# Kernel tuning notes

Hardware: AMD Instinct MI355X
Metric: run time of the kernel (lower is better)

## Reference

```python
import jax, jax.numpy as jnp
import numpy as np

B, S, H, L, NH, DH, FF = 64, 128, 768, 6, 12, 64, 3072
VOCAB, MAXPOS, INTENT, TAGS = 30522, 512, 22, 122
LN_EPS = 1e-12
INV_SQRT_DH = float(1.0 / np.sqrt(DH))


def _ln(x, s, b):
    m = x.mean(-1, keepdims=True)
    v = ((x - m) ** 2).mean(-1, keepdims=True)
    return (x - m) * jax.lax.rsqrt(v + LN_EPS) * s + b


def setup_inputs():
    key = jax.random.key(0)
    cnt = [0]
    def nk():
        cnt[0] += 1
        return jax.random.fold_in(key, cnt[0])
    def nrm(shape):
        return (0.02 * jax.random.normal(nk(), shape)).astype(jnp.float32)
    inp = {
        'input_ids': jax.random.randint(nk(), (B, S), 0, VOCAB),
        'attention_mask': jnp.ones((B, S), jnp.int32),
        'intent_target': jax.random.randint(nk(), (B,), 0, INTENT),
        'slots_target': jax.random.randint(nk(), (B, S), 0, TAGS),
        'slots_mask': jnp.ones((B, S), jnp.int32),
        'word_emb': nrm((VOCAB, H)), 'pos_emb': nrm((MAXPOS, H)),
        'emb_ln_s': jnp.ones((H,)), 'emb_ln_b': jnp.zeros((H,)),
        'Wq': nrm((L, H, H)), 'bq': jnp.zeros((L, H)),
        'Wk': nrm((L, H, H)), 'bk': jnp.zeros((L, H)),
        'Wv': nrm((L, H, H)), 'bv': jnp.zeros((L, H)),
        'Wo': nrm((L, H, H)), 'bo': jnp.zeros((L, H)),
        'sa_ln_s': jnp.ones((L, H)), 'sa_ln_b': jnp.zeros((L, H)),
        'W1f': nrm((L, H, FF)), 'b1f': jnp.zeros((L, FF)),
        'W2f': nrm((L, FF, H)), 'b2f': jnp.zeros((L, H)),
        'out_ln_s': jnp.ones((L, H)), 'out_ln_b': jnp.zeros((L, H)),
        'iW1': nrm((H, 64)), 'ib1': jnp.zeros((64,)),
        'iW2': nrm((64, INTENT)), 'ib2': jnp.zeros((INTENT,)),
        'sW1': nrm((H, 256)), 'sb1': jnp.zeros((256,)),
        'sW2': nrm((256, TAGS)), 'sb2': jnp.zeros((TAGS,)),
        'crf_start': nrm((TAGS,)), 'crf_end': nrm((TAGS,)), 'crf_trans': nrm((TAGS, TAGS)),
        'log_vars': jnp.zeros((2,)),
    }
    return inp


def _encoder(input_ids, attention_mask, word_emb, pos_emb, emb_ln_s, emb_ln_b,
             Wq, bq, Wk, bk, Wv, bv, Wo, bo, sa_ln_s, sa_ln_b,
             W1f, b1f, W2f, b2f, out_ln_s, out_ln_b):
    x = word_emb[input_ids] + pos_emb[jnp.arange(S)][None]
    x = _ln(x, emb_ln_s, emb_ln_b)
    neg = jnp.where(attention_mask[:, None, None, :] > 0, 0.0, -1e9).astype(x.dtype)
    for i in range(L):
        q = (x @ Wq[i] + bq[i]).reshape(B, S, NH, DH).transpose(0, 2, 1, 3)
        k = (x @ Wk[i] + bk[i]).reshape(B, S, NH, DH).transpose(0, 2, 1, 3)
        v = (x @ Wv[i] + bv[i]).reshape(B, S, NH, DH).transpose(0, 2, 1, 3)
        scores = jnp.einsum('bhqd,bhkd->bhqk', q, k) * INV_SQRT_DH + neg
        attn = jax.nn.softmax(scores, -1)
        ctx = jnp.einsum('bhqk,bhkd->bhqd', attn, v).transpose(0, 2, 1, 3).reshape(B, S, H)
        x = _ln(x + ctx @ Wo[i] + bo[i], sa_ln_s[i], sa_ln_b[i])
        h = jax.nn.gelu(x @ W1f[i] + b1f[i], approximate=False) @ W2f[i] + b2f[i]
        x = _ln(x + h, out_ln_s[i], out_ln_b[i])
    return x


def _crf_llh(emis, tags, mask, crf_start, crf_end, crf_trans):
    # pytorch-crf log-likelihood, reduction='sum'. emis [B,S,T], mask bool [B,S]
    fmask = mask.astype(emis.dtype)
    emit_sc = jnp.take_along_axis(emis, tags[..., None], -1)[..., 0]          # [B,S]
    trans_sc = crf_trans[tags[:, :-1], tags[:, 1:]]                            # [B,S-1]
    last_idx = mask.sum(1) - 1
    last_tag = tags[jnp.arange(B), last_idx]
    num = (crf_start[tags[:, 0]] + emit_sc[:, 0]
           + ((trans_sc + emit_sc[:, 1:]) * fmask[:, 1:]).sum(1)
           + crf_end[last_tag])
    def fstep(alpha, xs):
        emit_t, m_t = xs
        nxt = jax.nn.logsumexp(alpha[:, :, None] + crf_trans[None] + emit_t[:, None, :], axis=1)
        return jnp.where(m_t[:, None], nxt, alpha), None
    alpha0 = crf_start[None] + emis[:, 0]
    alpha, _ = jax.lax.scan(fstep, alpha0, (emis[:, 1:].transpose(1, 0, 2), mask[:, 1:].T))
    denom = jax.nn.logsumexp(alpha + crf_end[None], -1)
    return jnp.sum(num - denom)


def _viterbi(emis, mask, crf_start, crf_end, crf_trans):
    ident = jnp.arange(TAGS)[None, :]
    def vstep(alpha, xs):
        emit_t, m_t = xs
        score = alpha[:, :, None] + crf_trans[None] + emit_t[:, None, :]      # [B,T,T]
        bp = jnp.where(m_t[:, None], jnp.argmax(score, 1), ident)
        alpha = jnp.where(m_t[:, None], jnp.max(score, 1), alpha)
        return alpha, bp
    alpha0 = crf_start[None] + emis[:, 0]
    alpha, bps = jax.lax.scan(vstep, alpha0, (emis[:, 1:].transpose(1, 0, 2), mask[:, 1:].T))
    last = jnp.argmax(alpha + crf_end[None], -1)                               # [B]
    def bstep(tag, bp):
        prev = jnp.take_along_axis(bp, tag[:, None], 1)[:, 0]
        return prev, prev
    _, prevs = jax.lax.scan(bstep, last, bps, reverse=True)                    # [S-1,B]
    return jnp.concatenate([prevs, last[None]], 0).T                           # [B,S]


def reference(input_ids, attention_mask, intent_target, slots_target, slots_mask,
              word_emb, pos_emb, emb_ln_s, emb_ln_b,
              Wq, bq, Wk, bk, Wv, bv, Wo, bo, sa_ln_s, sa_ln_b,
              W1f, b1f, W2f, b2f, out_ln_s, out_ln_b,
              iW1, ib1, iW2, ib2, sW1, sb1, sW2, sb2,
              crf_start, crf_end, crf_trans, log_vars):
    x = _encoder(input_ids, attention_mask, word_emb, pos_emb, emb_ln_s, emb_ln_b,
                 Wq, bq, Wk, bk, Wv, bv, Wo, bo, sa_ln_s, sa_ln_b,
                 W1f, b1f, W2f, b2f, out_ln_s, out_ln_b)
    # intent head: linear1(relu(cls)) -> relu -> linear2 (dropout = eval identity)
    intent_logits = jax.nn.relu(jax.nn.relu(x[:, 0]) @ iW1 + ib1) @ iW2 + ib2
    intent_loss = (jax.nn.logsumexp(intent_logits, -1)
                   - jnp.take_along_axis(intent_logits, intent_target[:, None], 1)[:, 0])
    intent_pred = jnp.argmax(intent_logits, -1)
    # slots head
    slots_logits = jax.nn.relu(jax.nn.relu(x) @ sW1 + sb1) @ sW2 + sb2
    mask = slots_mask.astype(bool)
    slots_loss = -_crf_llh(slots_logits, slots_target, mask, crf_start, crf_end, crf_trans)
    p1 = jnp.exp(-log_vars[0])
    p2 = jnp.exp(-log_vars[1])
    joint_loss = jnp.sum(p1 * intent_loss + log_vars[0]) + (p2 * slots_loss + log_vars[1])
    slots_pred = _viterbi(slots_logits, mask, crf_start, crf_end, crf_trans)
    return joint_loss, slots_pred, intent_pred
```

## Files before the change

### kernel.cpp

```cpp
#include <hip/hip_runtime.h>
#include <math.h>
#include <stdint.h>

#define B_      64
#define S_      128
#define H_      768
#define L_      6
#define NH_     12
#define DH_     64
#define FF_     3072
#define INTENT_ 22
#define TAGS_   122
#define NT_     (B_*S_)
#define LN_EPS  1e-12f
#define INV_SQRT_DH 0.125f

#define GF_RELU_OUT 2
#define GF_GELU_OUT 4
#define GF_ADDRES   16
#define GF_ACCH     32

typedef _Float16 half8 __attribute__((ext_vector_type(8)));
typedef float    f32x4 __attribute__((ext_vector_type(4)));

// ... 209 lines not shown
            bfl[i] = *(const half8*)&Bl[n*32 + slot*8];
        }
        #pragma unroll
        for (int i = 0; i < 4; i++)
            #pragma unroll
            for (int j = 0; j < 4; j++) {
                acc[i][j] = __builtin_amdgcn_mfma_f32_16x16x32_f16(afh[i], bfh[j], acc[i][j], 0,0,0);
                acc[i][j] = __builtin_amdgcn_mfma_f32_16x16x32_f16(afh[i], bfl[j], acc[i][j], 0,0,0);
                acc[i][j] = __builtin_amdgcn_mfma_f32_16x16x32_f16(afl[i], bfh[j], acc[i][j], 0,0,0);
            }
        __syncthreads();
    }
    #pragma unroll
    for (int i = 0; i < 4; i++)
        #pragma unroll
        for (int j = 0; j < 4; j++)
            #pragma unroll
            for (int r = 0; r < 4; r++) {
                int gm = m0 + wm*64 + i*16 + quad*4 + r;
                int gn = n0 + wn*64 + j*16 + l15;
                float v = acc[i][j][r];
                if (bias) v += bias[gn];
                size_t ox = (size_t)gm*ldc + gn;
                if (flags & GF_ADDRES) {
                    size_t rx = (size_t)gm*ldr + gn;
                    v += (float)Rh[rx] + (float)Rl[rx];
                }
                if (flags & GF_ACCH)
                    v += (float)oh[ox] + (float)ol[ox];
                if (flags & GF_RELU_OUT) v = fmaxf(v, 0.f);
                if (flags & GF_GELU_OUT) v = 0.5f*v*(1.0f + erff(v*0.70710678118654752f));
                if (oh) {
                    _Float16 hv = (_Float16)v;
                    oh[ox] = hv;
                    ol[ox] = (_Float16)(v - (float)hv);
                } else {
                    C[ox] = v;
                }
            }
}

#define BM 64
#define BN 64
#define BK 16
__global__ __launch_bounds__(256) void gemm_kernel(
    const float* __restrict__ A, int lda,
    const float* __restrict__ W, int ldb,
    float* __restrict__ C, int ldc,
    const float* __restrict__ bias,
    int M, int N, int K)
{
    __shared__ __align__(16) float As[BK][BM+4];
    __shared__ __align__(16) float Bs[BK][BN+4];
    int tid = threadIdx.x;
    int tx = tid & 15, ty = tid >> 4;
    int m0 = blockIdx.x * BM;
    int n0 = blockIdx.y * BN;
    float acc[4][4] = {};
    for (int k0 = 0; k0 < K; k0 += BK) {
        #pragma unroll
        for (int r = 0; r < 4; r++) {
            int li = tid + 256*r;
            int m  = li >> 4;
            int kk = li & 15;
            int gm = m0 + m, gk = k0 + kk;
            As[kk][m] = (gm < M && gk < K) ? A[(size_t)gm*lda + gk] : 0.f;
        }
        #pragma unroll
        for (int r = 0; r < 4; r++) {
            int li = tid + 256*r;
            int kk = li >> 6;
            int n  = li & 63;
            int gk = k0 + kk, gn = n0 + n;
            Bs[kk][n] = (gk < K && gn < N) ? W[(size_t)gk*ldb + gn] : 0.f;
        }
        __syncthreads();
        #pragma unroll
        for (int kk = 0; kk < BK; kk++) {
            float4 a  = *(const float4*)&As[kk][ty*4];
            float4 bb = *(const float4*)&Bs[kk][tx*4];
            float av[4] = {a.x, a.y, a.z, a.w};
            float bv[4] = {bb.x, bb.y, bb.z, bb.w};
            #pragma unroll
            for (int i = 0; i < 4; i++)
                #pragma unroll
                for (int j = 0; j < 4; j++)
                    acc[i][j] += av[i] * bv[j];
        }
        __syncthreads();
    }
    #pragma unroll
    for (int i = 0; i < 4; i++) {
        int gm = m0 + ty*4 + i;
        if (gm >= M) continue;
        #pragma unroll
        for (int j = 0; j < 4; j++) {
            int gn = n0 + tx*4 + j;
            if (gn >= N) continue;
            float v = acc[i][j];
            if (bias) v += bias[gn];
            C[(size_t)gm*ldc + gn] = v;
        }
    }
}

__device__ inline int scidx(int row, int col) {
    return row*128 + (((col>>2) ^ (row&7))<<2) + (col&3);
}
__global__ __launch_bounds__(256) void attn2_kernel(
    const _Float16* __restrict__ QhG, const _Float16* __restrict__ QlG,
    const _Float16* __restrict__ KhG, const _Float16* __restrict__ KlG,
    const _Float16* __restrict__ VhG, const _Float16* __restrict__ VlG,
    const int* __restrict__ amask,
    _Float16* __restrict__ Ch, _Float16* __restrict__ Cl)
{
    __shared__ __align__(16) char smem[65536];
    _Float16* Qh_s = (_Float16*)smem;
    _Float16* Ql_s = Qh_s + 64*72;
    _Float16* Kh_s = Ql_s + 64*72;
    _Float16* Kl_s = Kh_s + 128*72;
    float*    Sc   = (float*)smem;
    _Float16* Vth  = (_Float16*)(smem + 32768);
    _Float16* Vtl  = Vth + 64*128;

    int blk = blockIdx.x;
    int qh2 = blk & 1;
    int bh  = blk >> 1;
    int b = bh / NH_, hh = bh % NH_;
    const int tid = threadIdx.x, lane = tid&63, wid = tid>>6;
    const int l15 = lane&15, quad = lane>>4;
    const int qr = wid*16;
    size_t tokb = (size_t)b*S_*H_ + (size_t)hh*DH_;

    float nmask[8];
    #pragma unroll
    for (int j = 0; j < 8; j++)
        nmask[j] = (amask[b*S_ + j*16 + l15] > 0) ? 0.f : -1e9f;

    {
        int row = tid>>2, part = (tid&3)*16;
        size_t qg = tokb + (size_t)(qh2*64 + row)*H_ + part;
        *(uint4*)&Qh_s[row*72 + part] = *(const uint4*)(QhG + qg);
        *(uint4*)&Ql_s[row*72 + part] = *(const uint4*)(QlG + qg);
        #pragma unroll
        for (int p = 0; p < 2; p++) {
            int krow = row + p*64;
            size_t kg = tokb + (size_t)krow*H_ + part;
            *(uint4*)&Kh_s[krow*72 + part] = *(const uint4*)(KhG + kg);
            *(uint4*)&Kl_s[krow*72 + part] = *(const uint4*)(KlG + kg);
        }
    }
    __syncthreads();

    f32x4 acc1[8];
    #pragma unroll
    for (int j = 0; j < 8; j++) acc1[j] = (f32x4){0.f,0.f,0.f,0.f};
    half8 aqh[2], aql[2];
    #pragma unroll
    for (int kc = 0; kc < 2; kc++) {
        aqh[kc] = *(const half8*)&Qh_s[(qr + l15)*72 + kc*32 + quad*8];
        aql[kc] = *(const half8*)&Ql_s[(qr + l15)*72 + kc*32 + quad*8];
    }
    #pragma unroll
    for (int j = 0; j < 8; j++) {
        #pragma unroll
        for (int kc = 0; kc < 2; kc++) {
            half8 bkh = *(const half8*)&Kh_s[(j*16 + l15)*72 + kc*32 + quad*8];
            half8 bkl = *(const half8*)&Kl_s[(j*16 + l15)*72 + kc*32 + quad*8];
            acc1[j] = __builtin_amdgcn_mfma_f32_16x16x32_f16(aqh[kc], bkh, acc1[j], 0,0,0);
            acc1[j] = __builtin_amdgcn_mfma_f32_16x16x32_f16(aqh[kc], bkl, acc1[j], 0,0,0);
            acc1[j] = __builtin_amdgcn_mfma_f32_16x16x32_f16(aql[kc], bkh, acc1[j], 0,0,0);
        }
    }
    __syncthreads();

    #pragma unroll
    for (int j = 0; j < 8; j++)
        #pragma unroll
        for (int r = 0; r < 4; r++) {
            int row = qr + quad*4 + r;
            int col = j*16 + l15;
            Sc[scidx(row, col)] = acc1[j][r]*INV_SQRT_DH + nmask[j];
        }
    {
        int key = tid>>1, dh = (tid&1)*32;
        union V32 { _Float16 h[32]; uint4 u[4]; } bufh, bufl;
        #pragma unroll
        for (int e = 0; e < 4; e++) {
            bufh.u[e] = *(const uint4*)(VhG + tokb + (size_t)key*H_ + dh + e*8);
            bufl.u[e] = *(const uint4*)(VlG + tokb + (size_t)key*H_ + dh + e*8);
        }
        int kg = key>>3, kr = key&7;
        #pragma unroll
        for (int e = 0; e < 32; e++) {
            int d = dh + e;
            int pos = kg ^ (d & 7);
            Vth[d*128 + pos*8 + kr] = bufh.h[e];
            Vtl[d*128 + pos*8 + kr] = bufl.h[e];
        }
    }
    __syncthreads();

    {
        int row = tid>>2, part = (tid&3)*32;
        float mx = -INFINITY;
        #pragma unroll 8
        for (int e = 0; e < 32; e++)
            mx = fmaxf(mx, Sc[scidx(row, part+e)]);
        mx = fmaxf(mx, __shfl_xor(mx, 1));
        mx = fmaxf(mx, __shfl_xor(mx, 2));
        float s = 0.f;
        #pragma unroll 8
        for (int e = 0; e < 32; e++) {
            int idx = scidx(row, part+e);
            float ev = expf(Sc[idx] - mx);
            Sc[idx] = ev; s += ev;
        }
        s += __shfl_xor(s, 1);
        s += __shfl_xor(s, 2);
        float inv = 1.0f / s;
        #pragma unroll 8
        for (int e = 0; e < 32; e++)
            Sc[scidx(row, part+e)] *= inv;
    }
    __syncthreads();

    f32x4 acc2[4];
    #pragma unroll
    for (int jd = 0; jd < 4; jd++) acc2[jd] = (f32x4){0.f,0.f,0.f,0.f};
    #pragma unroll
    for (int kc = 0; kc < 4; kc++) {
        int q = qr + l15;
        int g16 = kc*8 + quad*2;
        float4 p0 = *(const float4*)&Sc[q*128 + ((g16   ^ (q&7))<<2)];
        float4 p1 = *(const float4*)&Sc[q*128 + (((g16+1) ^ (q&7))<<2)];
        float pv[8] = {p0.x,p0.y,p0.z,p0.w, p1.x,p1.y,p1.z,p1.w};
        union U { _Float16 h[8]; half8 v; } ph, pl;
        #pragma unroll
        for (int e = 0; e < 8; e++) {
            _Float16 hv = (_Float16)pv[e];
            ph.h[e] = hv; pl.h[e] = (_Float16)(pv[e] - (float)hv);
        }
        #pragma unroll
        for (int jd = 0; jd < 4; jd++) {
            int n = jd*16 + l15;
            int pos = (kc*4 + quad) ^ (n & 7);
            half8 vh = *(const half8*)&Vth[n*128 + pos*8];
            half8 vl = *(const half8*)&Vtl[n*128 + pos*8];
            acc2[jd] = __builtin_amdgcn_mfma_f32_16x16x32_f16(ph.v, vh, acc2[jd], 0,0,0);
            acc2[jd] = __builtin_amdgcn_mfma_f32_16x16x32_f16(ph.v, vl, acc2[jd], 0,0,0);
            acc2[jd] = __builtin_amdgcn_mfma_f32_16x16x32_f16(pl.v, vh, acc2[jd], 0,0,0);
        }
    }
    #pragma unroll
    for (int jd = 0; jd < 4; jd++)
        #pragma unroll
        for (int r = 0; r < 4; r++) {
            int row = qr + quad*4 + r;
            int token = b*S_ + qh2*64 + row;
            int d = jd*16 + l15;
            float v = acc2[jd][r];
            _Float16 hv = (_Float16)v;
            Ch[(size_t)token*H_ + hh*DH_ + d] = hv;
            Cl[(size_t)token*H_ + hh*DH_ + d] = (_Float16)(v - (float)hv);
        }
}

__global__ __launch_bounds__(64) void intent_kernel(
    const _Float16* __restrict__ Xh, const _Float16* __restrict__ Xl,
    const float* __restrict__ iW1,
    const float* __restrict__ ib1, const float* __restrict__ iW2,
    const float* __restrict__ ib2, const int* __restrict__ tgt,
    float* __restrict__ iloss, float* __restrict__ outf)
{
    int b = blockIdx.x; int j = threadIdx.x;
    __shared__ float h1[64];
    __shared__ float lg[32];
    const _Float16* x0h = Xh + (size_t)b*S_*H_;
    const _Float16* x0l = Xl + (size_t)b*S_*H_;
    float acc = ib1[j];
    for (int h = 0; h < H_; h++) {
        float x = (float)x0h[h] + (float)x0l[h];
        acc += fmaxf(x, 0.f) * iW1[(size_t)h*64 + j];
    }
    h1[j] = fmaxf(acc, 0.f);
    __syncthreads();
    if (j < INTENT_) {
        float l = ib2[j];
        for (int k = 0; k < 64; k++) l += h1[k]*iW2[k*INTENT_ + j];
        lg[j] = l;
    }
    __syncthreads();
    if (j == 0) {
        float mx = -INFINITY; int bi = 0;
        for (int c = 0; c < INTENT_; c++) if (lg[c] > mx) { mx = lg[c]; bi = c; }
        float sm = 0.f;
        for (int c = 0; c < INTENT_; c++) sm += expf(lg[c]-mx);
        float lse = mx + logf(sm);
        iloss[b] = lse - lg[tgt[b]];
        outf[1 + (size_t)NT_ + b] = (float)bi;
    }
}

#define VST 130
__global__ __launch_bounds__(512) void crf_vit_kernel(
    const float* __restrict__ E_, const int* __restrict__ tags,
    const int* __restrict__ mask, const float* __restrict__ start,
    const float* __restrict__ endv, const float* __restrict__ trans,
    float* __restrict__ crfv, unsigned char* __restrict__ BPg,
    float* __restrict__ outf)
{
    __shared__ __align__(16) float tT[TAGS_*VST];
    __shared__ float alpha[TAGS_+2];
    __shared__ float ealpha[TAGS_+2];
    __shared__ float mxbuf[16];
    __shared__ int lastt;
    int b = blockIdx.x;
    int mode = blockIdx.y;
    int tid = threadIdx.x, lane = tid&63, wid = tid>>6;
    int j = tid>>2, p = tid&3;
    int cnt = (p < 2) ? 31 : 30;
    const float* E = E_ + (size_t)b*S_*TAGS_;

    if (j < TAGS_) {
        for (int e = 0; e < cnt; e++) {
            int i = 4*e + p;
            float tv = trans[i*TAGS_ + j];
            tT[j*VST + i] = mode ? tv : expf(tv);
        }
        if (p == 0) alpha[j] = start[j] + E[j];
    }
    __syncthreads();

    if (mode == 0) {
        for (int t = 1; t < S_; t++) {
            if (wid == 0) {
                float a = (lane < TAGS_) ? alpha[lane] : -3e38f;
                if (lane + 64 < TAGS_) a = fmaxf(a, alpha[lane+64]);
                a = wave_max(a);
                if (lane == 0) mxbuf[0] = a;
            }
            __syncthreads();
            float mx = mxbuf[0];
            if (p == 0 && j < TAGS_) ealpha[j] = expf(alpha[j] - mx);
            __syncthreads();
            float s = 0.f;
            if (j < TAGS_) {
                const float* tr = &tT[j*VST];
                for (int e = 0; e < cnt; e++) {
                    int i = 4*e + p;
                    s += ealpha[i]*tr[i];
                }
            }
            s += __shfl_xor(s, 1);
            s += __shfl_xor(s, 2);
            int m_t = mask[b*S_ + t];
            float ee = (j < TAGS_) ? E[(size_t)t*TAGS_ + j] : 0.f;
            float nv = mx + logf(s) + ee;
            __syncthreads();
            if (p == 0 && j < TAGS_ && m_t) alpha[j] = nv;
            __syncthreads();
        }
        float term = 0.f, mkf = 0.f;
        if (tid < S_) {
            int mk = mask[b*S_ + tid]; mkf = (float)mk;
            if (tid >= 1 && mk) {
                int tg = tags[b*S_ + tid], tgp = tags[b*S_ + tid - 1];
                term = trans[tgp*TAGS_ + tg] + E[(size_t)tid*TAGS_ + tg];
            }
        }
        if (wid < 2) {
            float ts = wave_sum(term);
            float ms = wave_sum(mkf);
            if (lane == 0) { mxbuf[2+wid] = ts; mxbuf[4+wid] = ms; }
        }
        __syncthreads();
        if (wid == 0) {
            float v1 = (lane < TAGS_) ? alpha[lane] + endv[lane] : -3e38f;
            float v2 = (lane+64 < TAGS_) ? alpha[lane+64] + endv[lane+64] : -3e38f;
            float m = wave_max(fmaxf(v1, v2));
            float sd = ((lane < TAGS_) ? expf(v1 - m) : 0.f)
                     + ((lane+64 < TAGS_) ? expf(v2 - m) : 0.f);
            sd = wave_sum(sd);
            if (lane == 0) {
                float denom = m + logf(sd);
                float numsum = mxbuf[2] + mxbuf[3];
                int msum = (int)(mxbuf[4] + mxbuf[5]);
                int tag0 = tags[b*S_];
                int last_tag = tags[b*S_ + (msum - 1)];
                float num = start[tag0] + E[tag0] + numsum + endv[last_tag];
                crfv[b] = num - denom;
            }
        }
    } else {
        size_t bpb = (size_t)b*(S_-1)*TAGS_;
        for (int t = 1; t < S_; t++) {
            float best = -3e38f; int bi = 0;
            if (j < TAGS_) {
                const float* tr = &tT[j*VST];
                for (int e = 0; e < cnt; e++) {
                    int i = 4*e + p;
                    float v = alpha[i] + tr[i];
                    if (v > best) { best = v; bi = i; }
                }
            }
            {
                float ov = __shfl_xor(best, 1); int oi = __shfl_xor(bi, 1);
                if (ov > best || (ov == best && oi < bi)) { best = ov; bi = oi; }
                ov = __shfl_xor(best, 2); oi = __shfl_xor(bi, 2);
                if (ov > best || (ov == best && oi < bi)) { best = ov; bi = oi; }
            }
            int m_t = mask[b*S_ + t];
            float ee = (j < TAGS_) ? E[(size_t)t*TAGS_ + j] : 0.f;
            float nv; int nb;
            if (m_t) { nv = best + ee; nb = bi; }
            else     { nv = (j < TAGS_) ? alpha[j] : 0.f; nb = j; }
            __syncthreads();
            if (p == 0 && j < TAGS_) {
                alpha[j] = nv;
                BPg[bpb + (size_t)(t-1)*TAGS_ + j] = (unsigned char)nb;
            }
            __syncthreads();
        }
        if (wid == 0) {
            float v; int idx;
            float v1 = (lane < TAGS_) ? alpha[lane] + endv[lane] : -3e38f;
            float v2 = (lane+64 < TAGS_) ? alpha[lane+64] + endv[lane+64] : -3e38f;
            if (v2 > v1) { v = v2; idx = lane+64; } else { v = v1; idx = lane; }
            #pragma unroll
            for (int d = 32; d; d >>= 1) {
                float ov = __shfl_xor(v, d); int oi = __shfl_xor(idx, d);
                if (ov > v || (ov == v && oi < idx)) { v = ov; idx = oi; }
            }
            if (lane == 0) lastt = idx;
        }
        __syncthreads();
        unsigned char* bpl = (unsigned char*)tT;
        for (int o = tid; o < (S_-1)*TAGS_; o += 512)
            bpl[o] = BPg[bpb + o];
        __syncthreads();
        if (tid == 0) {
            int tag = lastt;
            outf[1 + (size_t)b*S_ + (S_-1)] = (float)tag;
            for (int t = S_-1; t >= 1; t--) {
                tag = bpl[(t-1)*TAGS_ + tag];
                outf[1 + (size_t)b*S_ + (t-1)] = (float)tag;
            }
        }
    }
}

__global__ void combine_kernel(const float* __restrict__ iloss,
                               const float* __restrict__ crfv,
                               const float* __restrict__ lv,
                               float* __restrict__ outf)
{
    if (threadIdx.x == 0 && blockIdx.x == 0) {
        float si = 0.f, sc = 0.f;
        for (int b = 0; b < B_; b++) { si += iloss[b]; sc += crfv[b]; }
        float p1 = expf(-lv[0]), p2 = expf(-lv[1]);
        float slots_loss = -sc;
        outf[0] = p1*si + (float)B_*lv[0] + p2*slots_loss + lv[1];
    }
}

extern "C" void kernel_launch(void* const* d_in, const int* in_sizes, int n_in,
                              void* d_out, int out_size, void* d_ws, size_t ws_size,
                              hipStream_t stream) {
    const int*   ids   = (const int*)  d_in[0];
    const int*   amask = (const int*)  d_in[1];
    const int*   itgt  = (const int*)  d_in[2];
    const int*   stgt  = (const int*)  d_in[3];
    const int*   smask = (const int*)  d_in[4];
    const float* we    = (const float*)d_in[5];
    const float* pe    = (const float*)d_in[6];
    const float* embs  = (const float*)d_in[7];
    const float* embb  = (const float*)d_in[8];
    const float* Wq    = (const float*)d_in[9];
    const float* bq    = (const float*)d_in[10];
    const float* Wk    = (const float*)d_in[11];
    const float* bk    = (const float*)d_in[12];
    const float* Wv    = (const float*)d_in[13];
    const float* bv    = (const float*)d_in[14];
    const float* Wo    = (const float*)d_in[15];
    const float* bo    = (const float*)d_in[16];
    const float* sas   = (const float*)d_in[17];
    const float* sab   = (const float*)d_in[18];
    const float* W1f   = (const float*)d_in[19];
    const float* b1f   = (const float*)d_in[20];
    const float* W2f   = (const float*)d_in[21];
    const float* b2f   = (const float*)d_in[22];
    const float* ols   = (const float*)d_in[23];
    const float* olb   = (const float*)d_in[24];
    const float* iW1   = (const float*)d_in[25];
    const float* ib1   = (const float*)d_in[26];
    const float* iW2   = (const float*)d_in[27];
    const float* ib2   = (const float*)d_in[28];
    const float* sW1   = (const float*)d_in[29];
    const float* sb1   = (const float*)d_in[30];
    const float* sW2   = (const float*)d_in[31];
    const float* sb2   = (const float*)d_in[32];
    const float* crfs  = (const float*)d_in[33];
    const float* crfe  = (const float*)d_in[34];
    const float* crft  = (const float*)d_in[35];
    const float* lv    = (const float*)d_in[36];

    float* outf = (float*)d_out;
    float* wsf  = (float*)d_ws;
    const long NTHh = (long)NT_ * H_;
    const long NBf  = NTHh;
    const long HH   = (long)H_ * H_;

    _Float16* Xh = (_Float16*)wsf;
    _Float16* Xl = Xh + NTHh;
    float*    Pf = wsf + NBf;
    _Float16* Ph = (_Float16*)Pf;
    _Float16 *Qh = Ph, *Ql = Ph + NTHh, *Kh = Ph + 2*NTHh, *Kl = Ph + 3*NTHh,
             *Vh = Ph + 4*NTHh, *Vl = Ph + 5*NTHh;
    _Float16 *Sh = Ph, *Sl = Ph + NTHh;
    _Float16* Fh = (_Float16*)(wsf + 2*NBf);
    _Float16* Fl = (_Float16*)(wsf + 3*NBf);
    _Float16* Ch = (_Float16*)(wsf + 4*NBf);
    _Float16* Cl = Ch + NTHh;
    const long wa0 = 5*NBf;
    _Float16* WAh = (_Float16*)(wsf + wa0);
    _Float16* WAl = WAh + 4*HH;
    const long wb1 = wa0 + 2359296;
    _Float16* WB1h = (_Float16*)(wsf + wb1);
    _Float16* WB1l = WB1h + 2359296;
    const long wb2 = wb1 + 2359296;
    _Float16* WB2h = (_Float16*)(wsf + wb2);
    _Float16* WB2l = WB2h + 2359296;
    float* iloss = wsf + wb2 + 2359296;
    float* crfv  = iloss + 64;
    float* H1 = Pf;
    float* logits = Pf + 2097152;
    unsigned char* BPg = (unsigned char*)(Pf + 2097152 + 999424);

    auto g3 = [&](int gy, int gz,
                  const _Float16* A_h, const _Float16* A_l, int lda,
                  const _Float16* WtH, const _Float16* WtL, int ldw, long wz,
                  float* C, _Float16* OH, _Float16* OL, int ldc, long oz,
                  const _Float16* Rh, const _Float16* Rl,
                  const float* b0, const float* b1_, const float* b2_,
                  int K, int flags) {
        hipLaunchKernelGGL(gemm3_kernel, dim3(NT_/128, gy, gz), dim3(256), 0, stream,
                           A_h, A_l, lda, WtH, WtL, ldw, wz,
                           C, OH, OL, ldc, oz, Rh, Rl, H_, b0, b1_, b2_, K, flags);
    };

    hipLaunchKernelGGL(embed_ln_kernel, dim3(NT_), dim3(256), 0, stream,
                       ids, we, pe, embs, embb, Xh, Xl);

    for (int i = 0; i < L_; i++) {
        const long WO = (long)i*HH;
        hipLaunchKernelGGL(wconv_kernel, dim3(12,12,4), dim3(256), 0, stream,
                           Wq+WO, Wk+WO, Wv+WO, Wo+WO, H_, H_, WAh, WAl, HH);
        g3(6, 3, Xh, Xl, H_, WAh, WAl, H_, HH,
           nullptr, Ph, Ph+NTHh, H_, 2*NTHh, nullptr, nullptr,
           bq+i*H_, bk+i*H_, bv+i*H_, H_, 0);
        hipLaunchKernelGGL(attn2_kernel, dim3(B_*NH_*2), dim3(256), 0, stream,
                           Qh, Ql, Kh, Kl, Vh, Vl, amask, Ch, Cl);
        g3(6, 1, Ch, Cl, H_, WAh+3*HH, WAl+3*HH, H_, 0,
           nullptr, Sh, Sl, H_, 0, Xh, Xl,
           bo+i*H_, nullptr, nullptr, H_, GF_ADDRES);
        hipLaunchKernelGGL(ln2_kernel, dim3(NT_), dim3(384), 0, stream,
                           Sh, Sl, sas+i*H_, sab+i*H_, Xh, Xl,
                           (_Float16*)nullptr, (_Float16*)nullptr);
        hipLaunchKernelGGL(wconv_kernel, dim3(12,48,1), dim3(256), 0, stream,
                           W1f+(long)i*H_*FF_, nullptr, nullptr, nullptr,
                           H_, FF_, WB1h, WB1l, 0);
        hipLaunchKernelGGL(wconv_kernel, dim3(48,12,1), dim3(256), 0, stream,
                           W2f+(long)i*FF_*H_, nullptr, nullptr, nullptr,
                           FF_, H_, WB2h, WB2l, 0);
        for (int c = 0; c < 2; c++) {
            const int CW = FF_/2;
            g3(12, 1, Xh, Xl, H_,
               WB1h+(long)c*CW*H_, WB1l+(long)c*CW*H_, H_, 0,
               nullptr, Fh, Fl, CW, 0, nullptr, nullptr,
               b1f+(long)i*FF_+c*CW, nullptr, nullptr, H_, GF_GELU_OUT);
            g3(6, 1, Fh, Fl, CW,
               WB2h+(long)c*CW, WB2l+(long)c*CW, FF_, 0,
               nullptr, Sh, Sl, H_, 0, Xh, Xl,
               (c==0) ? (b2f+i*H_) : nullptr, nullptr, nullptr,
               CW, (c==0) ? GF_ADDRES : GF_ACCH);
        }
        hipLaunchKernelGGL(ln2_kernel, dim3(NT_), dim3(384), 0, stream,
                           Sh, Sl, ols+i*H_, olb+i*H_, Xh, Xl,
                           (i==L_-1) ? Ch : (_Float16*)nullptr,
                           (i==L_-1) ? Cl : (_Float16*)nullptr);
    }

    hipLaunchKernelGGL(intent_kernel, dim3(B_), dim3(64), 0, stream,
                       Xh, Xl, iW1, ib1, iW2, ib2, itgt, iloss, outf);

    hipLaunchKernelGGL(wconv_kernel, dim3(12,4,1), dim3(256), 0, stream,
                       sW1, nullptr, nullptr, nullptr, H_, 256,
                       WAh, WAh + (long)256*H_, 0);
    g3(2, 1, Ch, Cl, H_, WAh, WAh + (long)256*H_, H_, 0,
       H1, nullptr, nullptr, 256, 0, nullptr, nullptr,
       sb1, nullptr, nullptr, H_, GF_RELU_OUT);
    hipLaunchKernelGGL(gemm_kernel, dim3(NT_/BM, 2), dim3(256), 0, stream,
                       H1, 256, sW2, TAGS_, logits, TAGS_, sb2, NT_, TAGS_, 256);

    hipLaunchKernelGGL(crf_vit_kernel, dim3(B_, 2), dim3(512), 0, stream,
                       logits, stgt, smask, crfs, crfe, crft, crfv, BPg, outf);

    hipLaunchKernelGGL(combine_kernel, dim3(1), dim3(64), 0, stream,
                       iloss, crfv, lv, outf);
}
```

Baseline: 4.870 ms.

## Rewrite CRF/Viterbi kernel as single-wavefront with register-held alpha

The CRF forward and Viterbi kernel moves from 512 threads (4 lanes per tag with shared-memory alpha and several block barriers per timestep) to one 64-lane wavefront where each lane owns two tags in registers. Transitions are stored in an interleaved layout so each lane reads float4 values, and alpha is exchanged through a small LDS buffer without block barriers. This targets the serial per-timestep barrier and reduction overhead of the 127-step recurrence, at the cost of each lane doing the full 122-wide inner loop serially. Tie-breaking in the Viterbi argmax now depends on scan order instead of an explicit lowest-index rule.

```diff
diff --git a/kernel.cpp b/kernel.cpp
--- a/kernel.cpp
+++ b/kernel.cpp
@@ -535,145 +535,132 @@
     }
 }
 
-#define VST 130
-__global__ __launch_bounds__(512) void crf_vit_kernel(
+__global__ __launch_bounds__(64) void crf_vit_kernel(
     const float* __restrict__ E_, const int* __restrict__ tags,
     const int* __restrict__ mask, const float* __restrict__ start,
     const float* __restrict__ endv, const float* __restrict__ trans,
     float* __restrict__ crfv, unsigned char* __restrict__ BPg,
     float* __restrict__ outf)
 {
-    __shared__ __align__(16) float tT[TAGS_*VST];
-    __shared__ float alpha[TAGS_+2];
-    __shared__ float ealpha[TAGS_+2];
-    __shared__ float mxbuf[16];
-    __shared__ int lastt;
-    int b = blockIdx.x;
-    int mode = blockIdx.y;
-    int tid = threadIdx.x, lane = tid&63, wid = tid>>6;
-    int j = tid>>2, p = tid&3;
-    int cnt = (p < 2) ? 31 : 30;
+    __shared__ __align__(16) float Ti[61*256];
+    __shared__ __align__(16) float eab[128];
+    int b = blockIdx.x, mode = blockIdx.y;
+    int lane = threadIdx.x;
     const float* E = E_ + (size_t)b*S_*TAGS_;
-
-    if (j < TAGS_) {
-        for (int e = 0; e < cnt; e++) {
-            int i = 4*e + p;
-            float tv = trans[i*TAGS_ + j];
-            tT[j*VST + i] = mode ? tv : expf(tv);
-        }
-        if (p == 0) alpha[j] = start[j] + E[j];
-    }
-    __syncthreads();
+    int j0 = 2*lane, j1 = 2*lane+1;
+    bool vj0 = (j0 < TAGS_), vj1 = (j1 < TAGS_);
+
+    for (int o = lane; o < 61*256; o += 64) {
+        int i2 = o >> 8, r = o & 255, j = r >> 1, p = r & 1;
+        int i = 2*i2 + p;
+        float tv = (j < TAGS_) ? trans[i*TAGS_ + j] : 0.f;
+        Ti[o] = mode ? tv : expf(tv);
+    }
+    __syncthreads();
+
+    float a0 = vj0 ? (start[j0] + E[j0]) : -3e38f;
+    float a1 = vj1 ? (start[j1] + E[j1]) : -3e38f;
 
     if (mode == 0) {
         for (int t = 1; t < S_; t++) {
-            if (wid == 0) {
-                float a = (lane < TAGS_) ? alpha[lane] : -3e38f;
-                if (lane + 64 < TAGS_) a = fmaxf(a, alpha[lane+64]);
-                a = wave_max(a);
-                if (lane == 0) mxbuf[0] = a;
+            float e0 = vj0 ? E[(size_t)t*TAGS_ + j0] : 0.f;
+            float e1 = vj1 ? E[(size_t)t*TAGS_ + j1] : 0.f;
+            int m_t = mask[b*S_ + t];
+            float mx = wave_max(fmaxf(a0, a1));
+            float2 ea;
+            ea.x = vj0 ? expf(a0 - mx) : 0.f;
+            ea.y = vj1 ? expf(a1 - mx) : 0.f;
+            *(float2*)&eab[2*lane] = ea;
+            float s0 = 0.f, s1 = 0.f;
+            #pragma unroll
+            for (int i2 = 0; i2 < 61; i2++) {
+                float2 av = *(const float2*)&eab[2*i2];
+                float4 tv = *(const float4*)&Ti[i2*256 + 4*lane];
+                s0 += av.x*tv.x + av.y*tv.y;
+                s1 += av.x*tv.z + av.y*tv.w;
             }
-            __syncthreads();
-            float mx = mxbuf[0];
-            if (p == 0 && j < TAGS_) ealpha[j] = expf(alpha[j] - mx);
-            __syncthreads();
-            float s = 0.f;
-            if (j < TAGS_) {
-                const float* tr = &tT[j*VST];
-                for (int e = 0; e < cnt; e++) {
-                    int i = 4*e + p;
-                    s += ealpha[i]*tr[i];
-                }
+            if (m_t) {
+                if (vj0) a0 = mx + logf(s0) + e0;
+                if (vj1) a1 = mx + logf(s1) + e1;
             }
-            s += __shfl_xor(s, 1);
-            s += __shfl_xor(s, 2);
-            int m_t = mask[b*S_ + t];
-            float ee = (j < TAGS_) ? E[(size_t)t*TAGS_ + j] : 0.f;
-            float nv = mx + logf(s) + ee;
-            __syncthreads();
-            if (p == 0 && j < TAGS_ && m_t) alpha[j] = nv;
-            __syncthreads();
         }
         float term = 0.f, mkf = 0.f;
-        if (tid < S_) {
-            int mk = mask[b*S_ + tid]; mkf = (float)mk;
-            if (tid >= 1 && mk) {
-                int tg = tags[b*S_ + tid], tgp = tags[b*S_ + tid - 1];
-                term = trans[tgp*TAGS_ + tg] + E[(size_t)tid*TAGS_ + tg];
+        #pragma unroll
+        for (int rr = 0; rr < 2; rr++) {
+            int t = lane + 64*rr;
+            int mk = mask[b*S_ + t];
+            mkf += (float)mk;
+            if (t >= 1 && mk) {
+                int tg = tags[b*S_ + t], tgp = tags[b*S_ + t - 1];
+                term += trans[tgp*TAGS_ + tg] + E[(size_t)t*TAGS_ + tg];
             }
         }
-        if (wid < 2) {
-            float ts = wave_sum(term);
-            float ms = wave_sum(mkf);
-            if (lane == 0) { mxbuf[2+wid] = ts; mxbuf[4+wid] = ms; }
-        }
-        __syncthreads();
-        if (wid == 0) {
-            float v1 = (lane < TAGS_) ? alpha[lane] + endv[lane] : -3e38f;
-            float v2 = (lane+64 < TAGS_) ? alpha[lane+64] + endv[lane+64] : -3e38f;
-            float m = wave_max(fmaxf(v1, v2));
-            float sd = ((lane < TAGS_) ? expf(v1 - m) : 0.f)
-                     + ((lane+64 < TAGS_) ? expf(v2 - m) : 0.f);
-            sd = wave_sum(sd);
-            if (lane == 0) {
-                float denom = m + logf(sd);
-                float numsum = mxbuf[2] + mxbuf[3];
-                int msum = (int)(mxbuf[4] + mxbuf[5]);
-                int tag0 = tags[b*S_];
-                int last_tag = tags[b*S_ + (msum - 1)];
-                float num = start[tag0] + E[tag0] + numsum + endv[last_tag];
-                crfv[b] = num - denom;
-            }
+        float ts = wave_sum(term);
+        float ms = wave_sum(mkf);
+        float w0 = vj0 ? a0 + endv[j0] : -3e38f;
+        float w1 = vj1 ? a1 + endv[j1] : -3e38f;
+        float m2 = wave_max(fmaxf(w0, w1));
+        float sd = (vj0 ? expf(w0 - m2) : 0.f) + (vj1 ? expf(w1 - m2) : 0.f);
+        sd = wave_sum(sd);
+        if (lane == 0) {
+            float denom = m2 + logf(sd);
+            int msum = (int)ms;
+            int tag0 = tags[b*S_];
+            int last_tag = tags[b*S_ + (msum - 1)];
+            crfv[b] = start[tag0] + E[tag0] + ts + endv[last_tag] - denom;
         }
     } else {
         size_t bpb = (size_t)b*(S_-1)*TAGS_;
         for (int t = 1; t < S_; t++) {
-            float best = -3e38f; int bi = 0;
-            if (j < TAGS_) {
-                const float* tr = &tT[j*VST];
-                for (int e = 0; e < cnt; e++) {
-                    int i = 4*e + p;
-                    float v = alpha[i] + tr[i];
-                    if (v > best) { best = v; bi = i; }
+            float e0 = vj0 ? E[(size_t)t*TAGS_ + j0] : 0.f;
+            float e1 = vj1 ? E[(size_t)t*TAGS_ + j1] : 0.f;
+            int m_t = mask[b*S_ + t];
+            float2 ap; ap.x = a0; ap.y = a1;
+            *(float2*)&eab[2*lane] = ap;
+            float b0 = -3e38f, b1 = -3e38f; int i0 = 0, i1 = 0;
+            #pragma unroll
+            for (int i2 = 0; i2 < 61; i2++) {
+                float2 av = *(const float2*)&eab[2*i2];
+                float4 tv = *(const float4*)&Ti[i2*256 + 4*lane];
+                float c0 = av.x + tv.x;
+                if (c0 > b0) { b0 = c0; i0 = 2*i2; }
+                float c1 = av.y + tv.y;
+                if (c1 > b0) { b0 = c1; i0 = 2*i2+1; }
+                float c2 = av.x + tv.z;
+                if (c2 > b1) { b1 = c2; i1 = 2*i2; }
+                float c3 = av.y + tv.w;
+                if (c3 > b1) { b1 = c3; i1 = 2*i2+1; }
+            }
+            float n0, n1; int nb0, nb1;
+            if (m_t) { n0 = b0 + e0; nb0 = i0; n1 = b1 + e1; nb1 = i1; }
+            else     { n0 = a0; nb0 = j0; n1 = a1; nb1 = j1; }
+            if (vj0) a0 = n0;
+            if (vj1) a1 = n1;
+            if (vj0) {
+                size_t bx = bpb + (size_t)(t-1)*TAGS_ + j0;
+                if (vj1) {
+                    unsigned short pk = (unsigned short)(((nb1 & 0xff) << 8) | (nb0 & 0xff));
+                    *(unsigned short*)&BPg[bx] = pk;
+                } else {
+                    BPg[bx] = (unsigned char)nb0;
                 }
             }
-            {
-                float ov = __shfl_xor(best, 1); int oi = __shfl_xor(bi, 1);
-                if (ov > best || (ov == best && oi < bi)) { best = ov; bi = oi; }
-                ov = __shfl_xor(best, 2); oi = __shfl_xor(bi, 2);
-                if (ov > best || (ov == best && oi < bi)) { best = ov; bi = oi; }
-            }
-            int m_t = mask[b*S_ + t];
-            float ee = (j < TAGS_) ? E[(size_t)t*TAGS_ + j] : 0.f;
-            float nv; int nb;
-            if (m_t) { nv = best + ee; nb = bi; }
-            else     { nv = (j < TAGS_) ? alpha[j] : 0.f; nb = j; }
-            __syncthreads();
-            if (p == 0 && j < TAGS_) {
-                alpha[j] = nv;
-                BPg[bpb + (size_t)(t-1)*TAGS_ + j] = (unsigned char)nb;
-            }
-            __syncthreads();
-        }
-        if (wid == 0) {
-            float v; int idx;
-            float v1 = (lane < TAGS_) ? alpha[lane] + endv[lane] : -3e38f;
-            float v2 = (lane+64 < TAGS_) ? alpha[lane+64] + endv[lane+64] : -3e38f;
-            if (v2 > v1) { v = v2; idx = lane+64; } else { v = v1; idx = lane; }
-            #pragma unroll
-            for (int d = 32; d; d >>= 1) {
-                float ov = __shfl_xor(v, d); int oi = __shfl_xor(idx, d);
-                if (ov > v || (ov == v && oi < idx)) { v = ov; idx = oi; }
-            }
-            if (lane == 0) lastt = idx;
-        }
-        __syncthreads();
-        unsigned char* bpl = (unsigned char*)tT;
-        for (int o = tid; o < (S_-1)*TAGS_; o += 512)
+        }
+        float w0 = vj0 ? a0 + endv[j0] : -3e38f;
+        float w1 = vj1 ? a1 + endv[j1] : -3e38f;
+        float v = w0; int idx = j0;
+        if (w1 > v) { v = w1; idx = j1; }
+        #pragma unroll
+        for (int d = 32; d; d >>= 1) {
+            float ov = __shfl_xor(v, d); int oi = __shfl_xor(idx, d);
+            if (ov > v || (ov == v && oi < idx)) { v = ov; idx = oi; }
+        }
+        unsigned char* bpl = (unsigned char*)Ti;
+        for (int o = lane; o < (S_-1)*TAGS_; o += 64)
             bpl[o] = BPg[bpb + o];
         __syncthreads();
-        if (tid == 0) {
-            int tag = lastt;
+        if (lane == 0) {
+            int tag = idx;
             outf[1 + (size_t)b*S_ + (S_-1)] = (float)tag;
             for (int t = S_-1; t >= 1; t--) {
                 tag = bpl[(t-1)*TAGS_ + tag];
@@ -836,7 +823,7 @@
     hipLaunchKernelGGL(gemm_kernel, dim3(NT_/BM, 2), dim3(256), 0, stream,
                        H1, 256, sW2, TAGS_, logits, TAGS_, sb2, NT_, TAGS_, 256);
 
-    hipLaunchKernelGGL(crf_vit_kernel, dim3(B_, 2), dim3(512), 0, stream,
+    hipLaunchKernelGGL(crf_vit_kernel, dim3(B_, 2), dim3(64), 0, stream,
                        logits, stgt, smask, crfs, crfe, crft, crfv, BPg, outf);
 
     hipLaunchKernelGGL(combine_kernel, dim3(1), dim3(64), 0, stream,
```

After: 5.072 ms. 4.2% more time.

## Restructure CRF/Viterbi recurrence to one thread per tag with fewer barriers

Applied to the files above, without the earlier changes.

The CRF forward and Viterbi kernel now uses 128 threads, one per tag, instead of 512 threads with four partial-sum lanes per tag. Alpha is kept in registers and exchanged through a double-buffered shared array, which cuts each timestep to a single barrier. The running max is lagged by one step, and emissions and mask values are prefetched one step ahead. Each thread now performs a full 122-length dot or max per step using float4 loads, so per-thread work grows while synchronisation drops.

```diff
diff --git a/kernel.cpp b/kernel.cpp
--- a/kernel.cpp
+++ b/kernel.cpp
@@ -535,141 +535,164 @@
     }
 }
 
-#define VST 130
-__global__ __launch_bounds__(512) void crf_vit_kernel(
+#define VST 132
+__global__ __launch_bounds__(128) void crf_vit_kernel(
     const float* __restrict__ E_, const int* __restrict__ tags,
     const int* __restrict__ mask, const float* __restrict__ start,
     const float* __restrict__ endv, const float* __restrict__ trans,
     float* __restrict__ crfv, unsigned char* __restrict__ BPg,
     float* __restrict__ outf)
 {
-    __shared__ __align__(16) float tT[TAGS_*VST];
-    __shared__ float alpha[TAGS_+2];
-    __shared__ float ealpha[TAGS_+2];
-    __shared__ float mxbuf[16];
+    __shared__ __align__(16) float Ti[TAGS_*VST];
+    __shared__ __align__(16) float exbuf[2][128];
+    __shared__ float mxw[2][2];
+    __shared__ float red8[4];
     __shared__ int lastt;
-    int b = blockIdx.x;
-    int mode = blockIdx.y;
+    int b = blockIdx.x, mode = blockIdx.y;
     int tid = threadIdx.x, lane = tid&63, wid = tid>>6;
-    int j = tid>>2, p = tid&3;
-    int cnt = (p < 2) ? 31 : 30;
+    int j = tid;
+    bool vj = (j < TAGS_);
     const float* E = E_ + (size_t)b*S_*TAGS_;
 
-    if (j < TAGS_) {
-        for (int e = 0; e < cnt; e++) {
-            int i = 4*e + p;
-            float tv = trans[i*TAGS_ + j];
-            tT[j*VST + i] = mode ? tv : expf(tv);
-        }
-        if (p == 0) alpha[j] = start[j] + E[j];
-    }
-    __syncthreads();
+    for (int o = tid; o < TAGS_*VST; o += 128) {
+        int jj = o / VST, i = o - jj*VST;
+        float tv = (i < TAGS_) ? trans[i*TAGS_ + jj] : 0.f;
+        Ti[o] = mode ? tv : expf(tv);
+    }
+    float a = vj ? (start[j] + E[j]) : -3e38f;
 
     if (mode == 0) {
+        {
+            float wm = wave_max(a);
+            if (lane == 0) mxw[1][wid] = wm;
+        }
+        __syncthreads();
+        float mxP = fmaxf(mxw[1][0], mxw[1][1]);
+        float eC = vj ? E[(size_t)TAGS_ + j] : 0.f;
+        int   mC = mask[b*S_ + 1];
         for (int t = 1; t < S_; t++) {
-            if (wid == 0) {
-                float a = (lane < TAGS_) ? alpha[lane] : -3e38f;
-                if (lane + 64 < TAGS_) a = fmaxf(a, alpha[lane+64]);
-                a = wave_max(a);
-                if (lane == 0) mxbuf[0] = a;
-            }
+            int par = t & 1;
+            float e = eC; int m_t = mC;
+            if (t + 1 < S_) {
+                eC = vj ? E[(size_t)(t+1)*TAGS_ + j] : 0.f;
+                mC = mask[b*S_ + t + 1];
+            }
+            float ea = vj ? expf(a - mxP) : 0.f;
+            exbuf[par][tid] = ea;
+            float wm = wave_max(a);
+            if (lane == 0) mxw[par][wid] = wm;
             __syncthreads();
-            float mx = mxbuf[0];
-            if (p == 0 && j < TAGS_) ealpha[j] = expf(alpha[j] - mx);
-            __syncthreads();
-            float s = 0.f;
-            if (j < TAGS_) {
-                const float* tr = &tT[j*VST];
-                for (int e = 0; e < cnt; e++) {
-                    int i = 4*e + p;
-                    s += ealpha[i]*tr[i];
-                }
-            }
-            s += __shfl_xor(s, 1);
-            s += __shfl_xor(s, 2);
-            int m_t = mask[b*S_ + t];
-            float ee = (j < TAGS_) ? E[(size_t)t*TAGS_ + j] : 0.f;
-            float nv = mx + logf(s) + ee;
-            __syncthreads();
-            if (p == 0 && j < TAGS_ && m_t) alpha[j] = nv;
-            __syncthreads();
+            float mxC = fmaxf(mxw[par][0], mxw[par][1]);
+            const float* tr = &Ti[j*VST];
+            const float* eb = &exbuf[par][0];
+            float s0 = 0.f, s1 = 0.f, s2 = 0.f, s3 = 0.f;
+            #pragma unroll
+            for (int q = 0; q < 30; q++) {
+                float4 av = *(const float4*)&eb[q*4];
+                float4 tv = *(const float4*)&tr[q*4];
+                s0 += av.x*tv.x; s1 += av.y*tv.y;
+                s2 += av.z*tv.z; s3 += av.w*tv.w;
+            }
+            {
+                float2 av = *(const float2*)&eb[120];
+                float2 tv = *(const float2*)&tr[120];
+                s0 += av.x*tv.x; s1 += av.y*tv.y;
+            }
+            float s = (s0 + s1) + (s2 + s3);
+            if (m_t && vj) a = mxP + logf(s) + e;
+            mxP = mxC;
         }
         float term = 0.f, mkf = 0.f;
-        if (tid < S_) {
+        {
             int mk = mask[b*S_ + tid]; mkf = (float)mk;
             if (tid >= 1 && mk) {
                 int tg = tags[b*S_ + tid], tgp = tags[b*S_ + tid - 1];
                 term = trans[tgp*TAGS_ + tg] + E[(size_t)tid*TAGS_ + tg];
             }
         }
-        if (wid < 2) {
-            float ts = wave_sum(term);
-            float ms = wave_sum(mkf);
-            if (lane == 0) { mxbuf[2+wid] = ts; mxbuf[4+wid] = ms; }
-        }
-        __syncthreads();
-        if (wid == 0) {
-            float v1 = (lane < TAGS_) ? alpha[lane] + endv[lane] : -3e38f;
-            float v2 = (lane+64 < TAGS_) ? alpha[lane+64] + endv[lane+64] : -3e38f;
-            float m = wave_max(fmaxf(v1, v2));
-            float sd = ((lane < TAGS_) ? expf(v1 - m) : 0.f)
-                     + ((lane+64 < TAGS_) ? expf(v2 - m) : 0.f);
-            sd = wave_sum(sd);
-            if (lane == 0) {
-                float denom = m + logf(sd);
-                float numsum = mxbuf[2] + mxbuf[3];
-                int msum = (int)(mxbuf[4] + mxbuf[5]);
-                int tag0 = tags[b*S_];
-                int last_tag = tags[b*S_ + (msum - 1)];
-                float num = start[tag0] + E[tag0] + numsum + endv[last_tag];
-                crfv[b] = num - denom;
-            }
+        float ts = wave_sum(term);
+        float ms = wave_sum(mkf);
+        float w = vj ? a + endv[j] : -3e38f;
+        float wmx = wave_max(w);
+        if (lane == 0) { red8[wid] = wmx; mxw[0][wid] = ts; mxw[1][wid] = ms; }
+        __syncthreads();
+        float m2 = fmaxf(red8[0], red8[1]);
+        float sd = vj ? expf(w - m2) : 0.f;
+        sd = wave_sum(sd);
+        if (lane == 0) red8[2 + wid] = sd;
+        __syncthreads();
+        if (tid == 0) {
+            float denom = m2 + logf(red8[2] + red8[3]);
+            float tsum = mxw[0][0] + mxw[0][1];
+            int msum = (int)(mxw[1][0] + mxw[1][1]);
+            int tag0 = tags[b*S_];
+            int last_tag = tags[b*S_ + (msum - 1)];
+            crfv[b] = start[tag0] + E[tag0] + tsum + endv[last_tag] - denom;
         }
     } else {
+        __syncthreads();
         size_t bpb = (size_t)b*(S_-1)*TAGS_;
+        float eC = vj ? E[(size_t)TAGS_ + j] : 0.f;
+        int   mC = mask[b*S_ + 1];
         for (int t = 1; t < S_; t++) {
-            float best = -3e38f; int bi = 0;
-            if (j < TAGS_) {
-                const float* tr = &tT[j*VST];
-                for (int e = 0; e < cnt; e++) {
-                    int i = 4*e + p;
-                    float v = alpha[i] + tr[i];
-                    if (v > best) { best = v; bi = i; }
-                }
+            int par = t & 1;
+            float e = eC; int m_t = mC;
+            if (t + 1 < S_) {
+                eC = vj ? E[(size_t)(t+1)*TAGS_ + j] : 0.f;
+                mC = mask[b*S_ + t + 1];
+            }
+            exbuf[par][tid] = a;
+            __syncthreads();
+            const float* tr = &Ti[j*VST];
+            const float* ab = &exbuf[par][0];
+            float b0 = -3e38f, b1 = -3e38f, b2 = -3e38f, b3 = -3e38f;
+            int i0 = 0, i1 = 1, i2 = 2, i3 = 3;
+            #pragma unroll
+            for (int q = 0; q < 30; q++) {
+                float4 av = *(const float4*)&ab[q*4];
+                float4 tv = *(const float4*)&tr[q*4];
+                float c;
+                c = av.x + tv.x; if (c > b0) { b0 = c; i0 = q*4; }
+                c = av.y + tv.y; if (c > b1) { b1 = c; i1 = q*4+1; }
+                c = av.z + tv.z; if (c > b2) { b2 = c; i2 = q*4+2; }
+                c = av.w + tv.w; if (c > b3) { b3 = c; i3 = q*4+3; }
             }
             {
-                float ov = __shfl_xor(best, 1); int oi = __shfl_xor(bi, 1);
-                if (ov > best || (ov == best && oi < bi)) { best = ov; bi = oi; }
-                ov = __shfl_xor(best, 2); oi = __shfl_xor(bi, 2);
-                if (ov > best || (ov == best && oi < bi)) { best = ov; bi = oi; }
-            }
-            int m_t = mask[b*S_ + t];
-            float ee = (j < TAGS_) ? E[(size_t)t*TAGS_ + j] : 0.f;
+                float2 av = *(const float2*)&ab[120];
+                float2 tv = *(const float2*)&tr[120];
+                float c;
+                c = av.x + tv.x; if (c > b0) { b0 = c; i0 = 120; }
+                c = av.y + tv.y; if (c > b1) { b1 = c; i1 = 121; }
+            }
+            float bb = b0; int bi = i0;
+            if (b1 > bb || (b1 == bb && i1 < bi)) { bb = b1; bi = i1; }
+            if (b2 > bb || (b2 == bb && i2 < bi)) { bb = b2; bi = i2; }
+            if (b3 > bb || (b3 == bb && i3 < bi)) { bb = b3; bi = i3; }
             float nv; int nb;
-            if (m_t) { nv = best + ee; nb = bi; }
-            else     { nv = (j < TAGS_) ? alpha[j] : 0.f; nb = j; }
-            __syncthreads();
-            if (p == 0 && j < TAGS_) {
-                alpha[j] = nv;
+            if (m_t) { nv = bb + e; nb = bi; }
+            else     { nv = a; nb = j; }
+            if (vj) {
+                a = nv;
                 BPg[bpb + (size_t)(t-1)*TAGS_ + j] = (unsigned char)nb;
             }
-            __syncthreads();
-        }
-        if (wid == 0) {
-            float v; int idx;
-            float v1 = (lane < TAGS_) ? alpha[lane] + endv[lane] : -3e38f;
-            float v2 = (lane+64 < TAGS_) ? alpha[lane+64] + endv[lane+64] : -3e38f;
-            if (v2 > v1) { v = v2; idx = lane+64; } else { v = v1; idx = lane; }
-            #pragma unroll
-            for (int d = 32; d; d >>= 1) {
-                float ov = __shfl_xor(v, d); int oi = __shfl_xor(idx, d);
-                if (ov > v || (ov == v && oi < idx)) { v = ov; idx = oi; }
-            }
-            if (lane == 0) lastt = idx;
-        }
-        __syncthreads();
-        unsigned char* bpl = (unsigned char*)tT;
-        for (int o = tid; o < (S_-1)*TAGS_; o += 512)
+        }
+        float w = vj ? a + endv[j] : -3e38f;
+        float v = w; int idx = j;
+        #pragma unroll
+        for (int d = 32; d; d >>= 1) {
+            float ov = __shfl_xor(v, d); int oi = __shfl_xor(idx, d);
+            if (ov > v || (ov == v && oi < idx)) { v = ov; idx = oi; }
+        }
+        if (lane == 0) { red8[wid] = v; ((int*)&red8[2])[wid] = idx; }
+        __syncthreads();
+        if (tid == 0) {
+            float v0 = red8[0], v1 = red8[1];
+            int x0 = ((int*)&red8[2])[0], x1 = ((int*)&red8[2])[1];
+            lastt = (v1 > v0 || (v1 == v0 && x1 < x0)) ? x1 : x0;
+        }
+        __syncthreads();
+        unsigned char* bpl = (unsigned char*)Ti;
+        for (int o = tid; o < (S_-1)*TAGS_; o += 128)
             bpl[o] = BPg[bpb + o];
         __syncthreads();
         if (tid == 0) {
@@ -836,7 +859,7 @@
     hipLaunchKernelGGL(gemm_kernel, dim3(NT_/BM, 2), dim3(256), 0, stream,
                        H1, 256, sW2, TAGS_, logits, TAGS_, sb2, NT_, TAGS_, 256);
 
-    hipLaunchKernelGGL(crf_vit_kernel, dim3(B_, 2), dim3(512), 0, stream,
+    hipLaunchKernelGGL(crf_vit_kernel, dim3(B_, 2), dim3(128), 0, stream,
                        logits, stgt, smask, crfs, crfe, crft, crfv, BPg, outf);
 
     hipLaunchKernelGGL(combine_kernel, dim3(1), dim3(64), 0, stream,
```

After: 4.882 ms. About the same (+0.3%).

## Double-buffer CRF forward/Viterbi state to cut per-step block barriers

Applied to the files above, without the earlier changes.

Restructures the CRF forward and Viterbi loops so alpha lives in registers and is published into a ping-pong shared buffer. This cuts each timestep from four (or two) block barriers down to one, and computes the max for the next step's normalisation with per-wave reductions that every thread then combines. Emissions and mask values for the next step are prefetched, and the dot product is split across two accumulators. The stabilising max now lags one step behind, which relies on exp staying in range between steps and could hurt numerical robustness.

```diff
diff --git a/kernel.cpp b/kernel.cpp
--- a/kernel.cpp
+++ b/kernel.cpp
@@ -544,8 +544,8 @@
     float* __restrict__ outf)
 {
     __shared__ __align__(16) float tT[TAGS_*VST];
-    __shared__ float alpha[TAGS_+2];
-    __shared__ float ealpha[TAGS_+2];
+    __shared__ __align__(16) float eal[2][128];
+    __shared__ float mxw[2][8];
     __shared__ float mxbuf[16];
     __shared__ int lastt;
     int b = blockIdx.x;
@@ -553,47 +553,69 @@
     int tid = threadIdx.x, lane = tid&63, wid = tid>>6;
     int j = tid>>2, p = tid&3;
     int cnt = (p < 2) ? 31 : 30;
+    bool vj = (j < TAGS_);
     const float* E = E_ + (size_t)b*S_*TAGS_;
 
-    if (j < TAGS_) {
+    if (vj) {
         for (int e = 0; e < cnt; e++) {
             int i = 4*e + p;
             float tv = trans[i*TAGS_ + j];
             tT[j*VST + i] = mode ? tv : expf(tv);
         }
-        if (p == 0) alpha[j] = start[j] + E[j];
-    }
-    __syncthreads();
+    }
+    float aj = vj ? (start[j] + E[j]) : -3e38f;
 
     if (mode == 0) {
+        {
+            float wm = wave_max(aj);
+            if (lane == 0) mxw[0][wid] = wm;
+        }
+        __syncthreads();
+        float gm = mxw[0][0];
+        #pragma unroll
+        for (int w = 1; w < 8; w++) gm = fmaxf(gm, mxw[0][w]);
+        float xc = gm;
+        if (p == 0) eal[0][j] = vj ? expf(aj - xc) : 0.f;
+        __syncthreads();
+        int cur = 0;
+        float eC = vj ? E[(size_t)TAGS_ + j] : 0.f;
+        int   mC = mask[b*S_ + 1];
         for (int t = 1; t < S_; t++) {
-            if (wid == 0) {
-                float a = (lane < TAGS_) ? alpha[lane] : -3e38f;
-                if (lane + 64 < TAGS_) a = fmaxf(a, alpha[lane+64]);
-                a = wave_max(a);
-                if (lane == 0) mxbuf[0] = a;
-            }
-            __syncthreads();
-            float mx = mxbuf[0];
-            if (p == 0 && j < TAGS_) ealpha[j] = expf(alpha[j] - mx);
-            __syncthreads();
+            float e = eC; int m_t = mC;
+            if (t + 1 < S_) {
+                eC = vj ? E[(size_t)(t+1)*TAGS_ + j] : 0.f;
+                mC = mask[b*S_ + t + 1];
+            }
             float s = 0.f;
-            if (j < TAGS_) {
+            if (vj) {
                 const float* tr = &tT[j*VST];
-                for (int e = 0; e < cnt; e++) {
-                    int i = 4*e + p;
-                    s += ealpha[i]*tr[i];
+                const float* eb = &eal[cur][0];
+                float sa = 0.f, sb = 0.f;
+                for (int e2 = 0; e2 + 1 < cnt; e2 += 2) {
+                    int i0 = 4*e2 + p, i1 = 4*e2 + 4 + p;
+                    sa += eb[i0] * tr[i0];
+                    sb += eb[i1] * tr[i1];
                 }
+                if (cnt & 1) { int il = 4*(cnt-1) + p; sa += eb[il] * tr[il]; }
+                s = sa + sb;
             }
             s += __shfl_xor(s, 1);
             s += __shfl_xor(s, 2);
-            int m_t = mask[b*S_ + t];
-            float ee = (j < TAGS_) ? E[(size_t)t*TAGS_ + j] : 0.f;
-            float nv = mx + logf(s) + ee;
+            if (m_t && vj) aj = xc + logf(s) + e;
+            int nxt = cur ^ 1;
+            float xn = gm;
+            if (p == 0) eal[nxt][j] = vj ? expf(aj - xn) : 0.f;
+            float wm2 = wave_max(aj);
+            if (lane == 0) mxw[nxt][wid] = wm2;
             __syncthreads();
-            if (p == 0 && j < TAGS_ && m_t) alpha[j] = nv;
-            __syncthreads();
-        }
+            float nm = mxw[nxt][0];
+            #pragma unroll
+            for (int w = 1; w < 8; w++) nm = fmaxf(nm, mxw[nxt][w]);
+            gm = nm;
+            xc = xn;
+            cur = nxt;
+        }
+        if (p == 0) eal[0][j] = aj;
         float term = 0.f, mkf = 0.f;
         if (tid < S_) {
             int mk = mask[b*S_ + tid]; mkf = (float)mk;
@@ -609,8 +631,9 @@
         }
         __syncthreads();
         if (wid == 0) {
-            float v1 = (lane < TAGS_) ? alpha[lane] + endv[lane] : -3e38f;
-            float v2 = (lane+64 < TAGS_) ? alpha[lane+64] + endv[lane+64] : -3e38f;
+            const float* alp = &eal[0][0];
+            float v1 = (lane < TAGS_) ? alp[lane] + endv[lane] : -3e38f;
+            float v2 = (lane+64 < TAGS_) ? alp[lane+64] + endv[lane+64] : -3e38f;
             float m = wave_max(fmaxf(v1, v2));
             float sd = ((lane < TAGS_) ? expf(v1 - m) : 0.f)
                      + ((lane+64 < TAGS_) ? expf(v2 - m) : 0.f);
@@ -626,14 +649,25 @@
             }
         }
     } else {
+        if (p == 0) eal[0][j] = aj;
+        __syncthreads();
+        int cur = 0;
         size_t bpb = (size_t)b*(S_-1)*TAGS_;
+        float eC = vj ? E[(size_t)TAGS_ + j] : 0.f;
+        int   mC = mask[b*S_ + 1];
         for (int t = 1; t < S_; t++) {
+            float ee = eC; int m_t = mC;
+            if (t + 1 < S_) {
+                eC = vj ? E[(size_t)(t+1)*TAGS_ + j] : 0.f;
+                mC = mask[b*S_ + t + 1];
+            }
             float best = -3e38f; int bi = 0;
-            if (j < TAGS_) {
+            if (vj) {
                 const float* tr = &tT[j*VST];
+                const float* ab = &eal[cur][0];
                 for (int e = 0; e < cnt; e++) {
                     int i = 4*e + p;
-                    float v = alpha[i] + tr[i];
+                    float v = ab[i] + tr[i];
                     if (v > best) { best = v; bi = i; }
                 }
             }
@@ -643,22 +677,27 @@
                 ov = __shfl_xor(best, 2); oi = __shfl_xor(bi, 2);
                 if (ov > best || (ov == best && oi < bi)) { best = ov; bi = oi; }
             }
-            int m_t = mask[b*S_ + t];
-            float ee = (j < TAGS_) ? E[(size_t)t*TAGS_ + j] : 0.f;
             float nv; int nb;
             if (m_t) { nv = best + ee; nb = bi; }
-            else     { nv = (j < TAGS_) ? alpha[j] : 0.f; nb = j; }
+            else     { nv = aj; nb = j; }
+            int nxt = cur ^ 1;
+            if (vj) {
+                aj = nv;
+                if (p == 0) {
+                    eal[nxt][j] = aj;
+                    BPg[bpb + (size_t)(t-1)*TAGS_ + j] = (unsigned char)nb;
+                }
+            }
             __syncthreads();
-            if (p == 0 && j < TAGS_) {
-                alpha[j] = nv;
-                BPg[bpb + (size_t)(t-1)*TAGS_ + j] = (unsigned char)nb;
-            }
-            __syncthreads();
-        }
+            cur = nxt;
+        }
+        if (p == 0) eal[0][j] = aj;
+        __syncthreads();
         if (wid == 0) {
+            const float* alp = &eal[0][0];
             float v; int idx;
-            float v1 = (lane < TAGS_) ? alpha[lane] + endv[lane] : -3e38f;
-            float v2 = (lane+64 < TAGS_) ? alpha[lane+64] + endv[lane+64] : -3e38f;
+            float v1 = (lane < TAGS_) ? alp[lane] + endv[lane] : -3e38f;
+            float v2 = (lane+64 < TAGS_) ? alp[lane+64] + endv[lane+64] : -3e38f;
             if (v2 > v1) { v = v2; idx = lane+64; } else { v = v1; idx = lane; }
             #pragma unroll
             for (int d = 32; d; d >>= 1) {
```

Measured after the change: 4.808 ms. No clear change (-1.3%).
